# Kernel optimization log

Hardware: AMD Instinct MI355X
Metric: run time of the kernel (lower is better)

The kernel has to match this reference:

```python
import jax, jax.numpy as jnp
import numpy as np
import math


def setup_inputs() -> dict:
    key = jax.random.key(0)
    k1, k2, k3, k4 = jax.random.split(key, 4)
    B, L, H, D = 2, 4096, 8, 64
    factor = 5
    U = factor * int(np.ceil(np.log(L)))  # 45 = sample_k = n_top
    return {
        "queries": jax.random.normal(k1, (B, L, H, D), dtype=jnp.float32),
        "keys": jax.random.normal(k2, (B, L, H, D), dtype=jnp.float32),
        "values": jax.random.normal(k3, (B, L, H, D), dtype=jnp.float32),
        "index_sample": jax.random.randint(k4, (L, U), 0, L),  # sampled key ids per query
    }


def reference(queries, keys, values, index_sample):
    # ProbAttention forward, mask_flag=False (non-causal ProbSparse attention).
    B, L_Q, H, D = queries.shape
    L_K = keys.shape[1]
    Q = jnp.transpose(queries, (0, 2, 1, 3))  # (B,H,L_Q,D)
    K = jnp.transpose(keys, (0, 2, 1, 3))     # (B,H,L_K,D)
    V = jnp.transpose(values, (0, 2, 1, 3))   # (B,H,L_K,D)
    n_top = index_sample.shape[1]             # U = factor*ceil(ln(L_K)) = sample_k = n_top

    # --- _prob_QK: score each query against a random subset of keys ---
    K_sample = K[:, :, index_sample, :]                     # (B,H,L_Q,sample_k,D)
    Q_K_sample = jnp.einsum('bhqd,bhqsd->bhqs', Q, K_sample)
    # sparsity measure M = max - mean (sum divided by full L_K, as in source)
    M = Q_K_sample.max(-1) - Q_K_sample.sum(-1) / L_K       # (B,H,L_Q)
    _, M_top = jax.lax.top_k(M, n_top)                      # (B,H,n_top)

    # full attention scores only for the selected top queries
    Q_reduce = jnp.take_along_axis(Q, M_top[..., None], axis=2)  # (B,H,n_top,D)
    scale = 1.0 / math.sqrt(D)
    scores = jnp.einsum('bhud,bhkd->bhuk', Q_reduce, K) * scale  # (B,H,n_top,L_K)
    attn = jax.nn.softmax(scores, axis=-1)

    # --- initial context (mask_flag=False): cumulative sum of V ---
    context = jnp.cumsum(V, axis=2)                         # (B,H,L_Q,D)

    # --- scatter attention outputs into the top-query rows ---
    update = jnp.einsum('bhuk,bhkd->bhud', attn, V)         # (B,H,n_top,D)
    bi = jnp.arange(B)[:, None, None]
    hi = jnp.arange(H)[None, :, None]
    context = context.at[bi, hi, M_top].set(update)

    return jnp.transpose(context, (0, 2, 1, 3))             # (B,L_Q,H,D)
```

## Files before the change

kernel.cpp:

```cpp
#include <hip/hip_runtime.h>
#include <math.h>

#define BB 2
#define LL 4096
#define HH 8
#define DD 64
#define UU 45
#define TILE 128
#define NTILES (LL / TILE)

#define NC 64
#define CK (LL / NC)
#define KSTR 68
#define SSTR 68

__device__ __forceinline__ int qkv_idx(int b, int l, int h, int d) {
    return ((b * LL + l) * HH + h) * DD + d;
}

template <int CTRL>
__device__ __forceinline__ float dpp_add(float v) {
    int x = __builtin_amdgcn_update_dpp(0, __float_as_int(v), CTRL, 0xF, 0xF,
                                        true);
    return v + __int_as_float(x);
}

__global__ __launch_bounds__(256) void k_computeM(
        const float* __restrict__ Q, const float* __restrict__ K,
        const int* __restrict__ idx, float* __restrict__ M) {
    int w = (blockIdx.x * blockDim.x + threadIdx.x) >> 6;
    int lane = threadIdx.x & 63;
    int q = w % LL;
    int bh = w / LL;
    int h = bh % HH, b = bh / HH;

    const float* Kbh = K + (size_t)(b * LL * HH + h) * DD;
    const size_t rowStride = (size_t)HH * DD;

    int r = lane >> 4;
    int c16 = lane & 15;

    const float4 qf = *(const float4*)(Q + qkv_idx(b, q, h, c16 * 4));
    const int* idxRow = idx + q * UU;

    float mval = -INFINITY, sval = 0.f;
#pragma unroll
    for (int g = 0; g < 12; ++g) {
        int s = g * 4 + r;
        int ks = idxRow[s < UU ? s : 0];
        const float4* kp = (const float4*)(Kbh + (size_t)ks * rowStride);
        float4 kk = kp[c16];
        float part = fmaf(kk.x, qf.x,
                     fmaf(kk.y, qf.y, fmaf(kk.z, qf.z, kk.w * qf.w)));
        part = dpp_add<0x128>(part);
        part = dpp_add<0x124>(part);
        part = dpp_add<0x122>(part);
        part = dpp_add<0x121>(part);
        if (s < UU) { mval = fmaxf(mval, part); sval += part; }
    }
    mval = fmaxf(mval, __shfl_xor(mval, 16, 64));
    sval += __shfl_xor(sval, 16, 64);
    mval = fmaxf(mval, __shfl_xor(mval, 32, 64));
    sval += __shfl_xor(sval, 32, 64);
    if (lane == 0) M[bh * LL + q] = mval - sval * (1.0f / LL);
}

__global__ __launch_bounds__(1024) void k_topk(
        const float* __restrict__ M, int* __restrict__ Mtop,
        unsigned* __restrict__ selmap) {
    int bh = blockIdx.x;
    int t = threadIdx.x;
    __shared__ unsigned keys[LL];
    __shared__ unsigned hist[256];
    __shared__ unsigned scanbuf[256];
    __shared__ unsigned sPrefix, sMask, sK, sBin;
    __shared__ int outCount, eqCount;
    __shared__ int eqIdx[64];

    for (int i = t; i < LL; i += 1024) {
        unsigned u = __float_as_uint(M[bh * LL + i]);
        keys[i] = (u & 0x80000000u) ? ~u : (u | 0x80000000u);
    }
    if (selmap != nullptr && t < 128) selmap[bh * 128 + t] = 0u;
    if (t == 0) { sPrefix = 0u; sMask = 0u; sK = UU; outCount = 0; eqCount = 0; }
    __syncthreads();

    for (int pass = 0; pass < 4; ++pass) {
        int shift = 24 - pass * 8;
        if (t < 256) hist[t] = 0u;
        __syncthreads();
        unsigned prefix = sPrefix, mask = sMask;
        for (int i = t; i < LL; i += 1024) {
            unsigned k = keys[i];
            if ((k & mask) == prefix)
                atomicAdd(&hist[(k >> shift) & 0xFFu], 1u);
        }
        __syncthreads();
        if (t < 256) scanbuf[t] = hist[t];
        __syncthreads();
        for (int off = 1; off < 256; off <<= 1) {
            unsigned v = 0u;
            if (t < 256 && t + off < 256) v = scanbuf[t + off];
            __syncthreads();
            if (t < 256) scanbuf[t] += v;
            __syncthreads();
        }
        if (t < 256) {
            unsigned k = sK;
            unsigned geq = scanbuf[t];
            unsigned gt = (t < 255) ? scanbuf[t + 1] : 0u;
            if (gt < k && geq >= k) sBin = (unsigned)t;
        }
        __syncthreads();
        if (t == 0) {
            unsigned b = sBin;
            unsigned gt = (b < 255u) ? scanbuf[b + 1] : 0u;
            sK -= gt;
            sPrefix |= (b << shift);
            sMask |= (0xFFu << shift);
        }
        __syncthreads();
    }
    unsigned T = sPrefix;
    int kEq = (int)sK;

    for (int i = t; i < LL; i += 1024) {
        unsigned k = keys[i];
        if (k > T) {
            int slot = atomicAdd(&outCount, 1);
            Mtop[bh * UU + slot] = i;
        } else if (k == T) {
            int e = atomicAdd(&eqCount, 1);
            if (e < 64) eqIdx[e] = i;
        }
    }
    __syncthreads();

    if (t == 0) {
        int base = outCount;
        int ec = eqCount;
        if (ec <= 64) {
            for (int s = 0; s < UU; ++s) {
                if (s >= kEq) break;
                int bi = -1, bv = LL + 2;
                for (int j = 0; j < ec; ++j) {
                    int v = eqIdx[j];
                    if (v < bv) { bv = v; bi = j; }
                }
                Mtop[bh * UU + base + s] = bv;
                eqIdx[bi] = LL + 2;
            }
        } else {
            int got = 0;
            for (int i = 0; i < LL && got < kEq; ++i)
                if (keys[i] == T) { Mtop[bh * UU + base + got] = i; ++got; }
        }
    }
    __syncthreads();
    if (selmap != nullptr && t < UU) {
        int qi = Mtop[bh * UU + t];
        atomicOr(&selmap[bh * 128 + (qi >> 5)], 1u << (qi & 31));
    }
}

__global__ __launch_bounds__(256) void k_tilesum(
        const float* __restrict__ V, float* __restrict__ tsum) {
    int blk = blockIdx.x;
    int tile = blk % NTILES;
    int bh = blk / NTILES;
    int h = bh % HH, b = bh / HH;
    int d = threadIdx.x & 63, g = threadIdx.x >> 6;
    const int CH = TILE / 4;
    int l0 = tile * TILE + g * CH;
    float acc = 0.f;
    for (int i = 0; i < CH; ++i) acc += V[qkv_idx(b, l0 + i, h, d)];
    __shared__ float red[4][DD];
    red[g][d] = acc;
    __syncthreads();
    if (g == 0) tsum[blk * DD + d] = red[0][d] + red[1][d] + red[2][d] + red[3][d];
}

__global__ __launch_bounds__(256) void k_cumsum(
        const float* __restrict__ V, const float* __restrict__ tsum,
        const unsigned* __restrict__ selmap, float* __restrict__ out) {
    int blk = blockIdx.x;
    int tile = blk % NTILES;
    int bh = blk / NTILES;
    int h = bh % HH, b = bh / HH;
    int t = threadIdx.x;
    int d = t & 63, g = t >> 6;
    const int CH = TILE / 4;
    int l0 = tile * TILE + g * CH;

    __shared__ float red[4][DD];
    __shared__ float pre2[4][DD];
    float acc = 0.f;
    for (int i = 0; i < CH; ++i) acc += V[qkv_idx(b, l0 + i, h, d)];
    red[g][d] = acc;
    float p = 0.f;
    for (int tt = g; tt < tile; tt += 4)
        p += tsum[(bh * NTILES + tt) * DD + d];
    pre2[g][d] = p;
    __syncthreads();

    float off = pre2[0][d] + pre2[1][d] + pre2[2][d] + pre2[3][d];
    for (int gg = 0; gg < g; ++gg) off += red[gg][d];

    unsigned selw = (selmap != nullptr) ? selmap[bh * 128 + (l0 >> 5)] : 0u;

    float run = off;
    for (int i = 0; i < CH; ++i) {
        run += V[qkv_idx(b, l0 + i, h, d)];
        if (!((selw >> i) & 1u))
            out[qkv_idx(b, l0 + i, h, d)] = run;
    }
}

__global__ __launch_bounds__(256) void k_attn_partial(
        const float* __restrict__ Q, const float* __restrict__ K,
        const float* __restrict__ V, const int* __restrict__ Mtop,
        float* __restrict__ mPart, float* __restrict__ lPart,
        float* __restrict__ Op) {
    int blk = blockIdx.x;
    int c = blk % NC;
    int bh = blk / NC;
    int h = bh % HH, b = bh / HH;
    int k0 = c * CK;
    int t = threadIdx.x;

    __shared__ float Qs[48 * KSTR];
    __shared__ float Ks[CK * KSTR];
    __shared__ float Ss[UU * SSTR];

    const size_t rowStride = (size_t)HH * DD;
    const float* Qbh = Q + (size_t)(b * LL * HH + h) * DD;
    const float* Kbh = K + (size_t)(b * LL * HH + h) * DD;
    const float* Vbh = V + (size_t)(b * LL * HH + h) * DD;

    for (int p = t; p < 48 * DD; p += 256) {
        int u = p >> 6, d = p & 63;
        float v = 0.f;
        if (u < UU) {
            int qi = Mtop[bh * UU + u];
            v = Qbh[(size_t)qi * rowStride + d] * 0.125f;
        }
        Qs[u * KSTR + d] = v;
    }
    for (int p = t; p < CK * 16; p += 256) {
        int row = p >> 4, i = p & 15;
        *(float4*)&Ks[row * KSTR + i * 4] =
            *(const float4*)&Kbh[(size_t)(k0 + row) * rowStride + i * 4];
    }
    __syncthreads();

    int kq = t & 15, uq = t >> 4;
    int u0 = uq * 3;
    float acc[3][4];
#pragma unroll
    for (int i = 0; i < 3; ++i)
#pragma unroll
        for (int j = 0; j < 4; ++j) acc[i][j] = 0.f;

#pragma unroll 4
    for (int dd = 0; dd < 16; ++dd) {
        float4 qf[3];
#pragma unroll
        for (int i = 0; i < 3; ++i)
            qf[i] = *(const float4*)&Qs[(u0 + i) * KSTR + dd * 4];
        float4 kf[4];
#pragma unroll
        for (int j = 0; j < 4; ++j)
            kf[j] = *(const float4*)&Ks[(kq + 16 * j) * KSTR + dd * 4];
#pragma unroll
        for (int i = 0; i < 3; ++i)
#pragma unroll
            for (int j = 0; j < 4; ++j) {
                acc[i][j] = fmaf(qf[i].x, kf[j].x, acc[i][j]);
                acc[i][j] = fmaf(qf[i].y, kf[j].y, acc[i][j]);
                acc[i][j] = fmaf(qf[i].z, kf[j].z, acc[i][j]);
                acc[i][j] = fmaf(qf[i].w, kf[j].w, acc[i][j]);
            }
    }
#pragma unroll
    for (int i = 0; i < 3; ++i) {
        int u = u0 + i;
        if (u < UU)
#pragma unroll
            for (int j = 0; j < 4; ++j) Ss[u * SSTR + kq + 16 * j] = acc[i][j];
    }
    __syncthreads();

    for (int p = t; p < CK * 16; p += 256) {
        int row = p >> 4, i = p & 15;
        *(float4*)&Ks[row * KSTR + i * 4] =
            *(const float4*)&Vbh[(size_t)(k0 + row) * rowStride + i * 4];
    }

    if (t < UU * 4) {
        int u = t >> 2, qq = t & 3;
        float mloc = -INFINITY;
        for (int j = 0; j < CK / 4; ++j)
            mloc = fmaxf(mloc, Ss[u * SSTR + qq + 4 * j]);
        mloc = fmaxf(mloc, __shfl_xor(mloc, 1, 64));
        mloc = fmaxf(mloc, __shfl_xor(mloc, 2, 64));
        float lloc = 0.f;
        for (int j = 0; j < CK / 4; ++j) {
            int kk = qq + 4 * j;
            float e = __expf(Ss[u * SSTR + kk] - mloc);
            Ss[u * SSTR + kk] = e;
            lloc += e;
        }
        lloc += __shfl_xor(lloc, 1, 64);
        lloc += __shfl_xor(lloc, 2, 64);
        if (qq == 0) {
            mPart[(bh * NC + c) * UU + u] = mloc;
            lPart[(bh * NC + c) * UU + u] = lloc;
        }
    }
    __syncthreads();

    int dq = t & 15;
    int d0 = dq * 4;
    if (u0 < UU) {
        float4 o[3];
#pragma unroll
        for (int i = 0; i < 3; ++i) o[i] = make_float4(0.f, 0.f, 0.f, 0.f);
#pragma unroll 4
        for (int kc = 0; kc < CK / 4; ++kc) {
            float4 vk[4];
#pragma unroll
            for (int jj = 0; jj < 4; ++jj)
                vk[jj] = *(const float4*)&Ks[(4 * kc + jj) * KSTR + d0];
#pragma unroll
            for (int i = 0; i < 3; ++i) {
                float4 pf = *(const float4*)&Ss[(u0 + i) * SSTR + 4 * kc];
                o[i].x = fmaf(pf.x, vk[0].x, o[i].x);
                o[i].y = fmaf(pf.x, vk[0].y, o[i].y);
                o[i].z = fmaf(pf.x, vk[0].z, o[i].z);
                o[i].w = fmaf(pf.x, vk[0].w, o[i].w);
                o[i].x = fmaf(pf.y, vk[1].x, o[i].x);
                o[i].y = fmaf(pf.y, vk[1].y, o[i].y);
                o[i].z = fmaf(pf.y, vk[1].z, o[i].z);
                o[i].w = fmaf(pf.y, vk[1].w, o[i].w);
                o[i].x = fmaf(pf.z, vk[2].x, o[i].x);
                o[i].y = fmaf(pf.z, vk[2].y, o[i].y);
                o[i].z = fmaf(pf.z, vk[2].z, o[i].z);
                o[i].w = fmaf(pf.z, vk[2].w, o[i].w);
                o[i].x = fmaf(pf.w, vk[3].x, o[i].x);
                o[i].y = fmaf(pf.w, vk[3].y, o[i].y);
                o[i].z = fmaf(pf.w, vk[3].z, o[i].z);
                o[i].w = fmaf(pf.w, vk[3].w, o[i].w);
            }
        }
#pragma unroll
        for (int i = 0; i < 3; ++i) {
            int u = u0 + i;
            *(float4*)&Op[((size_t)(bh * NC + c) * UU + u) * DD + d0] = o[i];
        }
    }
}

__global__ void k_attn_combine(
        const int* __restrict__ Mtop, const float* __restrict__ mPart,
        const float* __restrict__ lPart, const float* __restrict__ Op,
        float* __restrict__ out) {
    int blk = blockIdx.x;
    int u = blk % UU;
    int bh = blk / UU;
    int h = bh % HH, b = bh / HH;
    int d = threadIdx.x;
    float gm = -INFINITY;
    for (int c = 0; c < NC; ++c)
        gm = fmaxf(gm, mPart[(bh * NC + c) * UU + u]);
    float denom = 0.f, acc = 0.f;
    for (int c = 0; c < NC; ++c) {
        int pi = (bh * NC + c) * UU + u;
        float w = __expf(mPart[pi] - gm);
        denom = fmaf(lPart[pi], w, denom);
        acc = fmaf(w, Op[(size_t)pi * DD + d], acc);
    }
    int qi = Mtop[bh * UU + u];
    out[qkv_idx(b, qi, h, d)] = acc / denom;
}

__global__ __launch_bounds__(256) void k_attn_mono(
        const float* __restrict__ Q, const float* __restrict__ K,
        const float* __restrict__ V, const int* __restrict__ Mtop,
        float* __restrict__ out) {
    int blk = blockIdx.x;
    int u = blk % UU;
    int bh = blk / UU;
    int h = bh % HH, b = bh / HH;
    int qi = Mtop[bh * UU + u];
    int t = threadIdx.x;

    __shared__ float scores[LL];
    __shared__ float red[256];

    const float4* qp = (const float4*)(Q + qkv_idx(b, qi, h, 0));
    float4 qreg[16];
#pragma unroll
    for (int i = 0; i < 16; ++i) {
        float4 v = qp[i];
        v.x *= 0.125f; v.y *= 0.125f; v.z *= 0.125f; v.w *= 0.125f;
        qreg[i] = v;
    }

    float lmax = -INFINITY;
    for (int k = t; k < LL; k += 256) {
        const float4* kr = (const float4*)(K + qkv_idx(b, k, h, 0));
        float dot = 0.f;
#pragma unroll
        for (int i = 0; i < 16; ++i) {
            float4 kk = kr[i];
            dot = fmaf(qreg[i].x, kk.x, dot);
            dot = fmaf(qreg[i].y, kk.y, dot);
            dot = fmaf(qreg[i].z, kk.z, dot);
            dot = fmaf(qreg[i].w, kk.w, dot);
        }
        scores[k] = dot;
        lmax = fmaxf(lmax, dot);
    }
    red[t] = lmax;
    __syncthreads();
    for (int off = 128; off >= 1; off >>= 1) {
        if (t < off) red[t] = fmaxf(red[t], red[t + off]);
        __syncthreads();
    }
    float smax = red[0];
    __syncthreads();

    float lsum = 0.f;
    for (int k = t; k < LL; k += 256) {
        float e = __expf(scores[k] - smax);
        scores[k] = e;
        lsum += e;
    }
    red[t] = lsum;
    __syncthreads();
    for (int off = 128; off >= 1; off >>= 1) {
        if (t < off) red[t] += red[t + off];
        __syncthreads();
    }
    float denom = red[0];
    __syncthreads();

    int d = t & 63, g = t >> 6;
    const float4* sc4 = (const float4*)scores;
    float acc = 0.f;
    for (int kb = g; kb < LL / 4; kb += 4) {
        float4 s4 = sc4[kb];
        int kk0 = kb * 4;
        acc = fmaf(s4.x, V[qkv_idx(b, kk0 + 0, h, d)], acc);
        acc = fmaf(s4.y, V[qkv_idx(b, kk0 + 1, h, d)], acc);
        acc = fmaf(s4.z, V[qkv_idx(b, kk0 + 2, h, d)], acc);
        acc = fmaf(s4.w, V[qkv_idx(b, kk0 + 3, h, d)], acc);
    }
    red[t] = acc;
    __syncthreads();
    if (g == 0) {
        float s = red[d] + red[64 + d] + red[128 + d] + red[192 + d];
        out[qkv_idx(b, qi, h, d)] = s / denom;
    }
}

extern "C" void kernel_launch(void* const* d_in, const int* in_sizes, int n_in,
                              void* d_out, int out_size, void* d_ws, size_t ws_size,
                              hipStream_t stream) {
    const float* Q = (const float*)d_in[0];
    const float* K = (const float*)d_in[1];
    const float* V = (const float*)d_in[2];
    const int* idx = (const int*)d_in[3];
    float* out = (float*)d_out;

    float* ws = (float*)d_ws;

    const size_t M_off = 0;
    const size_t tsum_off = 65536;
    const size_t mP_off = 98304;
    const size_t lP_off = 144384;
    const size_t top_off = 190464;
    const size_t sel_off = 191488;
    const size_t Op_off = 193536;
    const size_t need = (Op_off + (size_t)BB * HH * NC * UU * DD) * 4;

    float* M = ws + M_off;
    float* tsum = ws + tsum_off;

    if (ws_size >= need) {
        float* mPart = ws + mP_off;
        float* lPart = ws + lP_off;
        int* Mtop = (int*)(ws + top_off);
        unsigned* selmap = (unsigned*)(ws + sel_off);
        float* Op = ws + Op_off;

        k_computeM<<<BB * HH * LL / 4, 256, 0, stream>>>(Q, K, idx, M);
        k_topk<<<BB * HH, 1024, 0, stream>>>(M, Mtop, selmap);
        k_attn_partial<<<BB * HH * NC, 256, 0, stream>>>(Q, K, V, Mtop,
                                                         mPart, lPart, Op);
        k_tilesum<<<BB * HH * NTILES, 256, 0, stream>>>(V, tsum);
        k_attn_combine<<<BB * HH * UU, 64, 0, stream>>>(Mtop, mPart, lPart,
                                                        Op, out);
        k_cumsum<<<BB * HH * NTILES, 256, 0, stream>>>(V, tsum, selmap, out);
    } else {
        int* Mtop = (int*)(ws + 65536);
        float* tsum2 = ws + 65536 + 1024;
        k_computeM<<<BB * HH * LL / 4, 256, 0, stream>>>(Q, K, idx, M);
        k_topk<<<BB * HH, 1024, 0, stream>>>(M, Mtop, (unsigned*)nullptr);
        k_tilesum<<<BB * HH * NTILES, 256, 0, stream>>>(V, tsum2);
        k_cumsum<<<BB * HH * NTILES, 256, 0, stream>>>(V, tsum2,
                                                       (const unsigned*)nullptr,
                                                       out);
        k_attn_mono<<<BB * HH * UU, 256, 0, stream>>>(Q, K, V, Mtop, out);
    }
}
```

Measured before the change: 208.4 us.

## Merge tilesum into computeM launch and cumsum with combine to cut launches

```diff
diff --git a/kernel.cpp b/kernel.cpp
--- a/kernel.cpp
+++ b/kernel.cpp
@@ -14,6 +14,11 @@
 #define KSTR 68
 #define SSTR 68
 
+#define NB_CM (BB * HH * LL / 4)
+#define NB_TS (BB * HH * NTILES)
+#define NB_CU (BB * HH * NTILES)
+#define NB_CO (BB * HH * UU / 4)
+
 __device__ __forceinline__ int qkv_idx(int b, int l, int h, int d) {
     return ((b * LL + l) * HH + h) * DD + d;
 }
@@ -25,9 +30,28 @@
     return v + __int_as_float(x);
 }
 
-__global__ __launch_bounds__(256) void k_computeM(
+__global__ __launch_bounds__(256) void k_computeM_tilesum(
         const float* __restrict__ Q, const float* __restrict__ K,
-        const int* __restrict__ idx, float* __restrict__ M) {
+        const int* __restrict__ idx, const float* __restrict__ V,
+        float* __restrict__ M, float* __restrict__ tsum) {
+    if (blockIdx.x >= NB_CM) {
+        int blk = blockIdx.x - NB_CM;
+        int tile = blk % NTILES;
+        int bh = blk / NTILES;
+        int h = bh % HH, b = bh / HH;
+        int d = threadIdx.x & 63, g = threadIdx.x >> 6;
+        const int CH = TILE / 4;
+        int l0 = tile * TILE + g * CH;
+        float acc = 0.f;
+        for (int i = 0; i < CH; ++i) acc += V[qkv_idx(b, l0 + i, h, d)];
+        __shared__ float red[4][DD];
+        red[g][d] = acc;
+        __syncthreads();
+        if (g == 0)
+            tsum[blk * DD + d] =
+                red[0][d] + red[1][d] + red[2][d] + red[3][d];
+        return;
+    }
     int w = (blockIdx.x * blockDim.x + threadIdx.x) >> 6;
     int lane = threadIdx.x & 63;
     int q = w % LL;
@@ -43,20 +67,34 @@
     const float4 qf = *(const float4*)(Q + qkv_idx(b, q, h, c16 * 4));
     const int* idxRow = idx + q * UU;
 
-    float mval = -INFINITY, sval = 0.f;
+    int ks[12];
 #pragma unroll
     for (int g = 0; g < 12; ++g) {
         int s = g * 4 + r;
-        int ks = idxRow[s < UU ? s : 0];
-        const float4* kp = (const float4*)(Kbh + (size_t)ks * rowStride);
-        float4 kk = kp[c16];
-        float part = fmaf(kk.x, qf.x,
-                     fmaf(kk.y, qf.y, fmaf(kk.z, qf.z, kk.w * qf.w)));
-        part = dpp_add<0x128>(part);
-        part = dpp_add<0x124>(part);
-        part = dpp_add<0x122>(part);
-        part = dpp_add<0x121>(part);
-        if (s < UU) { mval = fmaxf(mval, part); sval += part; }
+        ks[g] = idxRow[s < UU ? s : 0];
+    }
+
+    float mval = -INFINITY, sval = 0.f;
+#pragma unroll
+    for (int half = 0; half < 2; ++half) {
+        float4 kk[6];
+#pragma unroll
+        for (int j = 0; j < 6; ++j)
+            kk[j] = ((const float4*)(Kbh +
+                        (size_t)ks[half * 6 + j] * rowStride))[c16];
+#pragma unroll
+        for (int j = 0; j < 6; ++j) {
+            int g = half * 6 + j;
+            float part = fmaf(kk[j].x, qf.x,
+                         fmaf(kk[j].y, qf.y,
+                         fmaf(kk[j].z, qf.z, kk[j].w * qf.w)));
+            part = dpp_add<0x128>(part);
+            part = dpp_add<0x124>(part);
+            part = dpp_add<0x122>(part);
+            part = dpp_add<0x121>(part);
+            int s = g * 4 + r;
+            if (s < UU) { mval = fmaxf(mval, part); sval += part; }
+        }
     }
     mval = fmaxf(mval, __shfl_xor(mval, 16, 64));
     sval += __shfl_xor(sval, 16, 64);
@@ -160,59 +198,6 @@
     if (selmap != nullptr && t < UU) {
         int qi = Mtop[bh * UU + t];
         atomicOr(&selmap[bh * 128 + (qi >> 5)], 1u << (qi & 31));
-    }
-}
-
-__global__ __launch_bounds__(256) void k_tilesum(
-        const float* __restrict__ V, float* __restrict__ tsum) {
-    int blk = blockIdx.x;
-    int tile = blk % NTILES;
-    int bh = blk / NTILES;
-    int h = bh % HH, b = bh / HH;
-    int d = threadIdx.x & 63, g = threadIdx.x >> 6;
-    const int CH = TILE / 4;
-    int l0 = tile * TILE + g * CH;
-    float acc = 0.f;
-    for (int i = 0; i < CH; ++i) acc += V[qkv_idx(b, l0 + i, h, d)];
-    __shared__ float red[4][DD];
-    red[g][d] = acc;
-    __syncthreads();
-    if (g == 0) tsum[blk * DD + d] = red[0][d] + red[1][d] + red[2][d] + red[3][d];
-}
-
-__global__ __launch_bounds__(256) void k_cumsum(
-        const float* __restrict__ V, const float* __restrict__ tsum,
-        const unsigned* __restrict__ selmap, float* __restrict__ out) {
-    int blk = blockIdx.x;
-    int tile = blk % NTILES;
-    int bh = blk / NTILES;
-    int h = bh % HH, b = bh / HH;
-    int t = threadIdx.x;
-    int d = t & 63, g = t >> 6;
-    const int CH = TILE / 4;
-    int l0 = tile * TILE + g * CH;
-
-    __shared__ float red[4][DD];
-    __shared__ float pre2[4][DD];
-    float acc = 0.f;
-    for (int i = 0; i < CH; ++i) acc += V[qkv_idx(b, l0 + i, h, d)];
-    red[g][d] = acc;
-    float p = 0.f;
-    for (int tt = g; tt < tile; tt += 4)
-        p += tsum[(bh * NTILES + tt) * DD + d];
-    pre2[g][d] = p;
-    __syncthreads();
-
-    float off = pre2[0][d] + pre2[1][d] + pre2[2][d] + pre2[3][d];
-    for (int gg = 0; gg < g; ++gg) off += red[gg][d];
-
-    unsigned selw = (selmap != nullptr) ? selmap[bh * 128 + (l0 >> 5)] : 0u;
-
-    float run = off;
-    for (int i = 0; i < CH; ++i) {
-        run += V[qkv_idx(b, l0 + i, h, d)];
-        if (!((selw >> i) & 1u))
-            out[qkv_idx(b, l0 + i, h, d)] = run;
     }
 }
 
@@ -360,27 +345,95 @@
     }
 }
 
-__global__ void k_attn_combine(
-        const int* __restrict__ Mtop, const float* __restrict__ mPart,
-        const float* __restrict__ lPart, const float* __restrict__ Op,
+__global__ __launch_bounds__(256) void k_cumsum_combine(
+        const float* __restrict__ V, const float* __restrict__ tsum,
+        const unsigned* __restrict__ selmap, const int* __restrict__ Mtop,
+        const float* __restrict__ mPart, const float* __restrict__ lPart,
+        const float* __restrict__ Op, float* __restrict__ out) {
+    int t = threadIdx.x;
+    if (blockIdx.x >= NB_CU) {
+        int u4 = (blockIdx.x - NB_CU) * 4 + (t >> 6);
+        int u = u4 % UU;
+        int bh = u4 / UU;
+        int h = bh % HH, b = bh / HH;
+        int d = t & 63;
+        float gm = -INFINITY;
+        for (int c = 0; c < NC; ++c)
+            gm = fmaxf(gm, mPart[(bh * NC + c) * UU + u]);
+        float denom = 0.f, acc = 0.f;
+        for (int c = 0; c < NC; ++c) {
+            int pi = (bh * NC + c) * UU + u;
+            float w = __expf(mPart[pi] - gm);
+            denom = fmaf(lPart[pi], w, denom);
+            acc = fmaf(w, Op[(size_t)pi * DD + d], acc);
+        }
+        int qi = Mtop[bh * UU + u];
+        out[qkv_idx(b, qi, h, d)] = acc / denom;
+        return;
+    }
+    int blk = blockIdx.x;
+    int tile = blk % NTILES;
+    int bh = blk / NTILES;
+    int h = bh % HH, b = bh / HH;
+    int d = t & 63, g = t >> 6;
+    const int CH = TILE / 4;
+    int l0 = tile * TILE + g * CH;
+
+    __shared__ float red[4][DD];
+    __shared__ float pre2[4][DD];
+    float acc = 0.f;
+    for (int i = 0; i < CH; ++i) acc += V[qkv_idx(b, l0 + i, h, d)];
+    red[g][d] = acc;
+    float p = 0.f;
+    for (int tt = g; tt < tile; tt += 4)
+        p += tsum[(bh * NTILES + tt) * DD + d];
+    pre2[g][d] = p;
+    __syncthreads();
+
+    float off = pre2[0][d] + pre2[1][d] + pre2[2][d] + pre2[3][d];
+    for (int gg = 0; gg < g; ++gg) off += red[gg][d];
+
+    unsigned selw = selmap[bh * 128 + (l0 >> 5)];
+
+    float run = off;
+    for (int i = 0; i < CH; ++i) {
+        run += V[qkv_idx(b, l0 + i, h, d)];
+        if (!((selw >> i) & 1u))
+            out[qkv_idx(b, l0 + i, h, d)] = run;
+    }
+}
+
+__global__ __launch_bounds__(256) void k_cumsum_fb(
+        const float* __restrict__ V, const float* __restrict__ tsum,
         float* __restrict__ out) {
     int blk = blockIdx.x;
-    int u = blk % UU;
-    int bh = blk / UU;
+    int tile = blk % NTILES;
+    int bh = blk / NTILES;
     int h = bh % HH, b = bh / HH;
-    int d = threadIdx.x;
-    float gm = -INFINITY;
-    for (int c = 0; c < NC; ++c)
-        gm = fmaxf(gm, mPart[(bh * NC + c) * UU + u]);
-    float denom = 0.f, acc = 0.f;
-    for (int c = 0; c < NC; ++c) {
-        int pi = (bh * NC + c) * UU + u;
-        float w = __expf(mPart[pi] - gm);
-        denom = fmaf(lPart[pi], w, denom);
-        acc = fmaf(w, Op[(size_t)pi * DD + d], acc);
-    }
-    int qi = Mtop[bh * UU + u];
-    out[qkv_idx(b, qi, h, d)] = acc / denom;
+    int t = threadIdx.x;
+    int d = t & 63, g = t >> 6;
+    const int CH = TILE / 4;
+    int l0 = tile * TILE + g * CH;
+
+    __shared__ float red[4][DD];
+    __shared__ float pre2[4][DD];
+    float acc = 0.f;
+    for (int i = 0; i < CH; ++i) acc += V[qkv_idx(b, l0 + i, h, d)];
+    red[g][d] = acc;
+    float p = 0.f;
+    for (int tt = g; tt < tile; tt += 4)
+        p += tsum[(bh * NTILES + tt) * DD + d];
+    pre2[g][d] = p;
+    __syncthreads();
+
+    float off = pre2[0][d] + pre2[1][d] + pre2[2][d] + pre2[3][d];
+    for (int gg = 0; gg < g; ++gg) off += red[gg][d];
+
+    float run = off;
+    for (int i = 0; i < CH; ++i) {
+        run += V[qkv_idx(b, l0 + i, h, d)];
+        out[qkv_idx(b, l0 + i, h, d)] = run;
+    }
 }
 
 __global__ __launch_bounds__(256) void k_attn_mono(
@@ -494,23 +547,20 @@
         unsigned* selmap = (unsigned*)(ws + sel_off);
         float* Op = ws + Op_off;
 
-        k_computeM<<<BB * HH * LL / 4, 256, 0, stream>>>(Q, K, idx, M);
+        k_computeM_tilesum<<<NB_CM + NB_TS, 256, 0, stream>>>(Q, K, idx, V,
+                                                              M, tsum);
         k_topk<<<BB * HH, 1024, 0, stream>>>(M, Mtop, selmap);
         k_attn_partial<<<BB * HH * NC, 256, 0, stream>>>(Q, K, V, Mtop,
                                                          mPart, lPart, Op);
-        k_tilesum<<<BB * HH * NTILES, 256, 0, stream>>>(V, tsum);
-        k_attn_combine<<<BB * HH * UU, 64, 0, stream>>>(Mtop, mPart, lPart,
-                                                        Op, out);
-        k_cumsum<<<BB * HH * NTILES, 256, 0, stream>>>(V, tsum, selmap, out);
+        k_cumsum_combine<<<NB_CU + NB_CO, 256, 0, stream>>>(
+            V, tsum, selmap, Mtop, mPart, lPart, Op, out);
     } else {
         int* Mtop = (int*)(ws + 65536);
         float* tsum2 = ws + 65536 + 1024;
-        k_computeM<<<BB * HH * LL / 4, 256, 0, stream>>>(Q, K, idx, M);
+        k_computeM_tilesum<<<NB_CM + NB_TS, 256, 0, stream>>>(Q, K, idx, V,
+                                                              M, tsum2);
         k_topk<<<BB * HH, 1024, 0, stream>>>(M, Mtop, (unsigned*)nullptr);
-        k_tilesum<<<BB * HH * NTILES, 256, 0, stream>>>(V, tsum2);
-        k_cumsum<<<BB * HH * NTILES, 256, 0, stream>>>(V, tsum2,
-                                                       (const unsigned*)nullptr,
-                                                       out);
+        k_cumsum_fb<<<BB * HH * NTILES, 256, 0, stream>>>(V, tsum2, out);
         k_attn_mono<<<BB * HH * UU, 256, 0, stream>>>(Q, K, V, Mtop, out);
     }
 }
```

After: 187.4 us. 1.11x faster.
